# Performance work log

Hardware: AMD Instinct MI355X
Metric: run time of the kernel (lower is better)

## Reference

```python
import jax, jax.numpy as jnp
import numpy as np

DIM = 1024
HIDDEN = 2816
NUM_EXPERTS = 8
TOP_K = 2
BATCH, SEQ = 4, 2048


def setup_inputs() -> dict:
    key = jax.random.key(0)
    ks = jax.random.split(key, 5)
    x = jax.random.normal(ks[0], (BATCH, SEQ, DIM), dtype=jnp.float32)
    gate_w = jax.random.normal(ks[1], (NUM_EXPERTS, DIM), dtype=jnp.float32) * 0.02
    w1 = jax.random.normal(ks[2], (NUM_EXPERTS, HIDDEN, DIM), dtype=jnp.float32) * 0.02
    w3 = jax.random.normal(ks[3], (NUM_EXPERTS, HIDDEN, DIM), dtype=jnp.float32) * 0.02
    w2 = jax.random.normal(ks[4], (NUM_EXPERTS, DIM, HIDDEN), dtype=jnp.float32) * 0.02
    return {"x": x, "gate_w": gate_w, "w1": w1, "w3": w3, "w2": w2}


def reference(x, gate_w, w1, w3, w2):
    orig_shape = x.shape
    xf = x.reshape(-1, x.shape[-1])                      # [T, D]
    T = xf.shape[0]
    E, K = gate_w.shape[0], TOP_K

    # gating: softmax over experts, then top-k (descending, matches torch.topk)
    scores = jax.nn.softmax(xf @ gate_w.T, axis=-1)      # [T, E]
    expert_weights, expert_indices = jax.lax.top_k(scores, K)  # [T, K]
    expert_weights = expert_weights / jnp.sum(expert_weights, axis=-1, keepdims=True)

    # dispatch: each token duplicated K times (torch repeat_interleave)
    x_rep = jnp.repeat(xf, K, axis=0)                    # [T*K, D]
    flat_idx = expert_indices.reshape(-1)                # [T*K]

    # per-expert masked SwiGLU FFN, combined into y (loop over small fixed E)
    y = jnp.zeros_like(x_rep)
    for e in range(E):
        m = (flat_idx == e)[:, None]
        xe = jnp.where(m, x_rep, 0.0)                    # zero non-routed tokens
        h = jax.nn.silu(xe @ w1[e].T) * (xe @ w3[e].T)   # [T*K, H]
        out = h @ w2[e].T                                # [T*K, D]
        y = y + jnp.where(m, out, 0.0)

    # weighted combine over the K slots
    y = jnp.sum(y.reshape(T, K, -1) * expert_weights[..., None], axis=1)
    return y.reshape(orig_shape)
```

## Files before the change

### kernel.cpp

```cpp
#include <hip/hip_runtime.h>
#include <hip/hip_bf16.h>

#define NTOK 8192
#define DIM 1024
#define HID 2816
#define NE 8
#define NSLOT (NTOK*2)
#define BM 128
#define BK 32
#define MAXMT (NSLOT/BM + NE)

typedef float f32x4 __attribute__((ext_vector_type(4)));
typedef __bf16 bf16x8 __attribute__((ext_vector_type(8)));
typedef __bf16 bf16x4 __attribute__((ext_vector_type(4)));

#define MFMA(a,b,c) __builtin_amdgcn_mfma_f32_16x16x32_bf16(a,b,c,0,0,0)
#define SWZ(r,g) (((r)<<5) + ((((g) ^ (((r)>>1)&3)))<<3))

__device__ __forceinline__ void cvt_st8(__bf16* d, f32x4 a, f32x4 b){
  bf16x8 v;
  v[0]=(__bf16)a.x; v[1]=(__bf16)a.y; v[2]=(__bf16)a.z; v[3]=(__bf16)a.w;
  v[4]=(__bf16)b.x; v[5]=(__bf16)b.y; v[6]=(__bf16)b.z; v[7]=(__bf16)b.w;
  *reinterpret_cast<bf16x8*>(d) = v;
}
__device__ __forceinline__ void gld_lds16(const void* g, void* l){
  __builtin_amdgcn_global_load_lds(
    (const __attribute__((address_space(1))) void*)g,
    (__attribute__((address_space(3))) void*)l, 16, 0, 0);
}
__device__ __forceinline__ int xcd_map(int orig, int nwg){
  int q = nwg>>3, rr = nwg&7, x = orig&7, o = orig>>3;
  return (x<rr ? x*(q+1) : rr*(q+1)+(x-rr)*q) + o;
}

__global__ void k_zero(int* cnt){ if(threadIdx.x < NE) cnt[threadIdx.x] = 0; }

__global__ __launch_bounds__(256) void k_cvt3(
    const float* __restrict__ s1, const float* __restrict__ s3,
    const float* __restrict__ s2, __bf16* __restrict__ d1,
    __bf16* __restrict__ d3, __bf16* __restrict__ d2)
{
  const int PB = (NE*HID*DIM/8)/256;
  int seg = blockIdx.x / PB;
  int i   = (blockIdx.x % PB)*256 + threadIdx.x;
  const float* src = (seg==0) ? s1 : (seg==1) ? s3 : s2;
  __bf16*      dst = (seg==0) ? d1 : (seg==1) ? d3 : d2;
  const f32x4* s = reinterpret_cast<const f32x4*>(src) + (size_t)i*2;
  f32x4 a = s[0], b = s[1];
  cvt_st8(dst + (size_t)i*8, a, b);
}

__global__ __launch_bounds__(256) void k_gate(const float* __restrict__ x,
    const float* __restrict__ gw, int* __restrict__ idxs,
    float* __restrict__ wt, int* __restrict__ cnt, __bf16* __restrict__ xb)
{
  __shared__ double part[8][8][4];
  __shared__ double lg[8][8];

  int tid = threadIdx.x;
  int tl = tid>>5, e = (tid>>2)&7, q = tid&3;
  int t  = blockIdx.x*8 + tl;

  const f32x4* x4 = reinterpret_cast<const f32x4*>(x)  + (size_t)t*256 + q*64;
  const f32x4* g4 = reinterpret_cast<const f32x4*>(gw) + e*256 + q*64;

  double s0 = 0.0, s1 = 0.0;
#pragma unroll 4
  for(int j=0;j<64;j+=2){
    f32x4 a0 = x4[j],   b0 = g4[j];
    f32x4 a1 = x4[j+1], b1 = g4[j+1];
    s0 += (double)a0.x*b0.x + (double)a0.y*b0.y
        + (double)a0.z*b0.z + (double)a0.w*b0.w;
    s1 += (double)a1.x*b1.x + (double)a1.y*b1.y
        + (double)a1.z*b1.z + (double)a1.w*b1.w;
  }
  part[tl][e][q] = s0 + s1;
  __syncthreads();
  if(q==0)
    lg[tl][e] = part[tl][e][0] + part[tl][e][1] + part[tl][e][2] + part[tl][e][3];
  __syncthreads();

  if(tid < 8){
    int tt = blockIdx.x*8 + tid;
    int i1=0; double m1=lg[tid][0];
#pragma unroll
    for(int k=1;k<NE;k++) if(lg[tid][k]>m1){ m1=lg[tid][k]; i1=k; }
    int i2=-1; double m2=-1e300;
#pragma unroll
    for(int k=0;k<NE;k++) if(k!=i1 && lg[tid][k]>m2){ m2=lg[tid][k]; i2=k; }
    float e2 = __expf((float)(m2-m1));
    float w0 = 1.f/(1.f+e2);
    idxs[2*tt]=i1; idxs[2*tt+1]=i2;
    wt[2*tt]=w0;   wt[2*tt+1]=e2*w0;
    atomicAdd(&cnt[i1],1); atomicAdd(&cnt[i2],1);
  }

  const f32x4* xs = reinterpret_cast<const f32x4*>(x) + (size_t)blockIdx.x*2048;
  __bf16* xo = xb + (size_t)blockIdx.x*8192;
#pragma unroll
  for(int k=0;k<4;k++){
    int c = k*256 + tid;
    cvt_st8(xo + (size_t)c*8, xs[2*c], xs[2*c+1]);
  }
}

__global__ void k_prep(const int* __restrict__ cnt, int* __restrict__ off,
                       int* __restrict__ mtp, int* __restrict__ cursor)
{
  if(threadIdx.x==0){
    int o=0, m=0; off[0]=0; mtp[0]=0;
    for(int e=0;e<NE;e++){
      cursor[e]=o; o += cnt[e]; off[e+1]=o;
      m += (cnt[e]+BM-1)/BM;  mtp[e+1]=m;
    }
  }
}

__global__ __launch_bounds__(256) void k_scatter(const int* __restrict__ idxs,
    int* __restrict__ cursor, int* __restrict__ order, int* __restrict__ inv)
{
  int t = blockIdx.x*blockDim.x + threadIdx.x;
#pragma unroll
  for(int k=0;k<2;k++){
    int s = 2*t+k;
    int e = idxs[s];
    int p = atomicAdd(&cursor[e],1);
    order[p]=s; inv[s]=p;
  }
}

__global__ __launch_bounds__(512) void k_ffn1(
    const __bf16* __restrict__ xb, const __bf16* __restrict__ w1b,
    const __bf16* __restrict__ w3b, const int* __restrict__ off,
    const int* __restrict__ mtp, const int* __restrict__ order,
    __bf16* __restrict__ h)
{
  __shared__ __align__(16) __bf16 lA [2][BM*BK];
  __shared__ __align__(16) __bf16 lB1[2][BM*BK];
  __shared__ __align__(16) __bf16 lB3[2][BM*BK];

  const int NT = HID/128;
  int wg = xcd_map(blockIdx.x, MAXMT*NT);
  int mt = wg / NT, nt = wg % NT;
  if (mt >= mtp[NE]) return;
  int e = 0;
  while (mt >= mtp[e+1]) e++;
  int row0    = off[e] + (mt - mtp[e])*BM;
  int row_end = off[e+1];
  int n0      = nt*128;

  int tid = threadIdx.x, lane = tid&63;
  int srow = tid>>2;
  int scol = ((tid&3) ^ ((srow>>1)&3))<<3;
  int arow = min(row0 + srow, row_end-1);
  int tok  = order[arow] >> 1;
  const __bf16* gA  = xb  + (size_t)tok*DIM + scol;
  const __bf16* gB1 = w1b + (size_t)e*HID*DIM + (size_t)(n0+srow)*DIM + scol;
  const __bf16* gB3 = w3b + (size_t)e*HID*DIM + (size_t)(n0+srow)*DIM + scol;
  int ldso = (tid>>6)<<9;

  int wm = (tid>>6)>>2, wn = (tid>>6)&3;
  int fr = lane & 15, gq = lane>>4;

  f32x4 acc1[4][2], acc3[4][2];
#pragma unroll
  for(int m=0;m<4;m++)
#pragma unroll
    for(int n=0;n<2;n++){ acc1[m][n]=f32x4{0.f,0.f,0.f,0.f}; acc3[m][n]=f32x4{0.f,0.f,0.f,0.f}; }

  gld_lds16(gA,  &lA [0][ldso]);
  gld_lds16(gB1, &lB1[0][ldso]);
  gld_lds16(gB3, &lB3[0][ldso]);
  __syncthreads();

  const int NK = DIM/BK;
  int buf=0;
  for(int kt=0; kt<NK; kt++){
    if(kt+1<NK){
      gld_lds16(gA  + (kt+1)*BK, &lA [buf^1][ldso]);
      gld_lds16(gB1 + (kt+1)*BK, &lB1[buf^1][ldso]);
      gld_lds16(gB3 + (kt+1)*BK, &lB3[buf^1][ldso]);
    }
    bf16x8 av[4], bv[2], cv[2];
#pragma unroll
    for(int m=0;m<4;m++) av[m]=*reinterpret_cast<const bf16x8*>(&lA[buf][SWZ(wm*64+m*16+fr, gq)]);
#pragma unroll
    for(int n=0;n<2;n++){
      bv[n]=*reinterpret_cast<const bf16x8*>(&lB1[buf][SWZ(wn*32+n*16+fr, gq)]);
      cv[n]=*reinterpret_cast<const bf16x8*>(&lB3[buf][SWZ(wn*32+n*16+fr, gq)]);
    }
#pragma unroll
    for(int m=0;m<4;m++)
#pragma unroll
      for(int n=0;n<2;n++){
        acc1[m][n]=MFMA(av[m],bv[n],acc1[m][n]);
        acc3[m][n]=MFMA(av[m],cv[n],acc3[m][n]);
      }
    __syncthreads();
    buf^=1;
  }

#pragma unroll
  for(int m=0;m<4;m++){
    int rbase = row0 + wm*64 + m*16 + (gq<<2);
#pragma unroll
    for(int r=0;r<4;r++){
      if(rbase+r < row_end){
        __bf16* hp = h + (size_t)(rbase+r)*HID + n0 + wn*32 + fr;
#pragma unroll
        for(int n=0;n<2;n++){
          float u = acc1[m][n][r], v = acc3[m][n][r];
          hp[n*16] = (__bf16)( (u/(1.f+__expf(-u))) * v );
        }
      }
    }
  }
}

__global__ __launch_bounds__(256) void k_ffn2(
    const __bf16* __restrict__ h, const __bf16* __restrict__ w2b,
    const int* __restrict__ off, const int* __restrict__ mtp,
    __bf16* __restrict__ ys)
{
  __shared__ __align__(16) __bf16 lA[2][128*BK];
  __shared__ __align__(16) __bf16 lB[2][128*BK];

  const int NT = DIM/128;
  int wg = xcd_map(blockIdx.x, MAXMT*NT);
  int mt = wg / NT, nt = wg % NT;
  if (mt >= mtp[NE]) return;
  int e = 0;
  while (mt >= mtp[e+1]) e++;
  int row0    = off[e] + (mt - mtp[e])*BM;
  int row_end = off[e+1];
  int n0      = nt*128;

  int tid = threadIdx.x, lane = tid&63, wave = tid>>6;
  int srow = tid>>2;
  int scol = ((tid&3) ^ ((srow>>1)&3))<<3;
  int hr0 = min(row0 + srow,      NSLOT-1);
  int hr1 = min(row0 + srow + 64, NSLOT-1);
  const __bf16* gA0 = h   + (size_t)hr0*HID + scol;
  const __bf16* gA1 = h   + (size_t)hr1*HID + scol;
  const __bf16* gB0 = w2b + (size_t)e*DIM*HID + (size_t)(n0+srow)*HID + scol;
  const __bf16* gB1 = w2b + (size_t)e*DIM*HID + (size_t)(n0+srow+64)*HID + scol;
  int ldso = wave<<9;

  int wm = wave>>1, wn = wave&1;
  int fr = lane&15, gq = lane>>4;

  f32x4 acc[4][4];
#pragma unroll
  for(int m=0;m<4;m++)
#pragma unroll
    for(int n=0;n<4;n++) acc[m][n]=f32x4{0.f,0.f,0.f,0.f};

  gld_lds16(gA0, &lA[0][ldso]);
  gld_lds16(gA1, &lA[0][2048+ldso]);
  gld_lds16(gB0, &lB[0][ldso]);
  gld_lds16(gB1, &lB[0][2048+ldso]);
  __syncthreads();

  const int NK = HID/BK;
  int buf=0;
  for(int kt=0; kt<NK; kt++){
    if(kt+1<NK){
      gld_lds16(gA0 + (kt+1)*BK, &lA[buf^1][ldso]);
      gld_lds16(gA1 + (kt+1)*BK, &lA[buf^1][2048+ldso]);
      gld_lds16(gB0 + (kt+1)*BK, &lB[buf^1][ldso]);
      gld_lds16(gB1 + (kt+1)*BK, &lB[buf^1][2048+ldso]);
    }
    bf16x8 av[4], bv[4];
#pragma unroll
    for(int m=0;m<4;m++) av[m]=*reinterpret_cast<const bf16x8*>(&lA[buf][SWZ(wm*64+m*16+fr, gq)]);
#pragma unroll
    for(int n=0;n<4;n++) bv[n]=*reinterpret_cast<const bf16x8*>(&lB[buf][SWZ(wn*64+n*16+fr, gq)]);
#pragma unroll
    for(int m=0;m<4;m++)
#pragma unroll
      for(int n=0;n<4;n++)
        acc[m][n]=MFMA(av[m],bv[n],acc[m][n]);
    __syncthreads();
    buf^=1;
  }

#pragma unroll
  for(int m=0;m<4;m++){
    int rbase = row0 + wm*64 + m*16 + (gq<<2);
#pragma unroll
    for(int r=0;r<4;r++){
      if(rbase+r < row_end){
        __bf16* yp = ys + (size_t)(rbase+r)*DIM + n0 + wn*64 + fr;
#pragma unroll
        for(int n=0;n<4;n++) yp[n*16] = (__bf16)acc[m][n][r];
      }
    }
  }
}

__global__ __launch_bounds__(256) void k_combine(
    const __bf16* __restrict__ ys, const int* __restrict__ inv,
    const float* __restrict__ wt, float* __restrict__ y)
{
  int t  = blockIdx.x;
  int p0 = inv[2*t], p1 = inv[2*t+1];
  float w0 = wt[2*t], w1v = wt[2*t+1];
  int d = threadIdx.x*4;
  const __bf16* r0 = ys + (size_t)p0*DIM + d;
  const __bf16* r1 = ys + (size_t)p1*DIM + d;
  f32x4 o;
#pragma unroll
  for(int j=0;j<4;j++) o[j] = w0*(float)r0[j] + w1v*(float)r1[j];
  *reinterpret_cast<f32x4*>(y + (size_t)t*DIM + d) = o;
}

extern "C" void kernel_launch(void* const* d_in, const int* in_sizes, int n_in,
                              void* d_out, int out_size, void* d_ws, size_t ws_size,
                              hipStream_t stream)
{
  const float* x  = (const float*)d_in[0];
  const float* gw = (const float*)d_in[1];
  const float* w1 = (const float*)d_in[2];
  const float* w3 = (const float*)d_in[3];
  const float* w2 = (const float*)d_in[4];
  float* y = (float*)d_out;
  char* ws = (char*)d_ws;

  int*   cnt    = (int*)(ws + 0);
  int*   off    = (int*)(ws + 64);
  int*   mtp    = (int*)(ws + 128);
  int*   cursor = (int*)(ws + 256);
  int*   idxs   = (int*)(ws + 320);
  float* wt     = (float*)(ws + 320 + 65536);
  int*   order  = (int*)(ws + 320 + 2*65536);
  int*   inv    = (int*)(ws + 320 + 3*65536);
  __bf16* h     = (__bf16*)(ws + 262464);
  __bf16* xb    = (__bf16*)(ws + 262464 + 92274688ull);
  __bf16* w1b   = (__bf16*)(ws + 262464 + 92274688ull + 16777216ull);
  __bf16* w3b   = (__bf16*)(ws + 262464 + 92274688ull + 16777216ull + 46137344ull);
  __bf16* w2b   = (__bf16*)(ws + 262464 + 92274688ull + 16777216ull + 2*46137344ull);
  __bf16* ysb   = w1b;

  const int PB = (NE*HID*DIM/8)/256;

  k_zero   <<<1, 64, 0, stream>>>(cnt);
  k_gate   <<<NTOK/8, 256, 0, stream>>>(x, gw, idxs, wt, cnt, xb);
  k_prep   <<<1, 64, 0, stream>>>(cnt, off, mtp, cursor);
  k_scatter<<<NTOK/256, 256, 0, stream>>>(idxs, cursor, order, inv);
  k_cvt3   <<<3*PB, 256, 0, stream>>>(w1, w3, w2, w1b, w3b, w2b);
  k_ffn1   <<<MAXMT*(HID/128), 512, 0, stream>>>(xb, w1b, w3b, off, mtp, order, h);
  k_ffn2   <<<MAXMT*(DIM/128), 256, 0, stream>>>(h, w2b, off, mtp, ysb);
  k_combine<<<NTOK, 256, 0, stream>>>(ysb, inv, wt, y);
}
```

Before: 644.1 us.

## Triple-buffer ffn2 K-loop with vmcnt waits and split ffn1 into two launches

The down-projection GEMM moves from a double-buffered LDS pipeline with a full __syncthreads per step to a three-stage ring. It keeps two tile loads in flight and waits with s_waitcnt vmcnt plus a single barrier, so global-to-LDS latency can overlap more of the MFMA work. The gate/up GEMM is also split into two launches that each cover half of the 22 hidden column tiles, which changes workgroup ordering and L2 reuse of the expert weights. The ring adds LDS use in ffn2 and depends on hand-tuned waitcnt counts being correct, and the extra launch adds overhead.

```diff
diff --git a/kernel.cpp b/kernel.cpp
--- a/kernel.cpp
+++ b/kernel.cpp
@@ -16,6 +16,7 @@
 
 #define MFMA(a,b,c) __builtin_amdgcn_mfma_f32_16x16x32_bf16(a,b,c,0,0,0)
 #define SWZ(r,g) (((r)<<5) + ((((g) ^ (((r)>>1)&3)))<<3))
+#define VMW(N) asm volatile("s_waitcnt vmcnt(" #N ")" ::: "memory")
 
 __device__ __forceinline__ void cvt_st8(__bf16* d, f32x4 a, f32x4 b){
   bf16x8 v;
@@ -129,19 +130,19 @@
   }
 }
 
+#define NT_H 11
 __global__ __launch_bounds__(512) void k_ffn1(
     const __bf16* __restrict__ xb, const __bf16* __restrict__ w1b,
     const __bf16* __restrict__ w3b, const int* __restrict__ off,
     const int* __restrict__ mtp, const int* __restrict__ order,
-    __bf16* __restrict__ h)
+    __bf16* __restrict__ h, int nt_off)
 {
   __shared__ __align__(16) __bf16 lA [2][BM*BK];
   __shared__ __align__(16) __bf16 lB1[2][BM*BK];
   __shared__ __align__(16) __bf16 lB3[2][BM*BK];
 
-  const int NT = HID/128;
-  int wg = xcd_map(blockIdx.x, MAXMT*NT);
-  int mt = wg / NT, nt = wg % NT;
+  int wg = xcd_map(blockIdx.x, MAXMT*NT_H);
+  int mt = wg / NT_H, nt = nt_off + wg % NT_H;
   if (mt >= mtp[NE]) return;
   int e = 0;
   while (mt >= mtp[e+1]) e++;
@@ -222,8 +223,8 @@
     const int* __restrict__ off, const int* __restrict__ mtp,
     __bf16* __restrict__ ys)
 {
-  __shared__ __align__(16) __bf16 lA[2][128*BK];
-  __shared__ __align__(16) __bf16 lB[2][128*BK];
+  __shared__ __align__(16) __bf16 lA[3][128*BK];
+  __shared__ __align__(16) __bf16 lB[3][128*BK];
 
   const int NT = DIM/128;
   int wg = xcd_map(blockIdx.x, MAXMT*NT);
@@ -255,34 +256,39 @@
 #pragma unroll
     for(int n=0;n<4;n++) acc[m][n]=f32x4{0.f,0.f,0.f,0.f};
 
-  gld_lds16(gA0, &lA[0][ldso]);
-  gld_lds16(gA1, &lA[0][2048+ldso]);
-  gld_lds16(gB0, &lB[0][ldso]);
-  gld_lds16(gB1, &lB[0][2048+ldso]);
-  __syncthreads();
+#define F2_STG(b, kt_) { \
+    gld_lds16(gA0 + (kt_)*BK, &lA[b][ldso]); \
+    gld_lds16(gA1 + (kt_)*BK, &lA[b][2048+ldso]); \
+    gld_lds16(gB0 + (kt_)*BK, &lB[b][ldso]); \
+    gld_lds16(gB1 + (kt_)*BK, &lB[b][2048+ldso]); }
+
+#define F2_CMP(b) { \
+    bf16x8 av[4], bv[4]; \
+    _Pragma("unroll") for(int m_=0;m_<4;m_++) \
+      av[m_]=*reinterpret_cast<const bf16x8*>(&lA[b][SWZ(wm*64+m_*16+fr, gq)]); \
+    _Pragma("unroll") for(int n_=0;n_<4;n_++) \
+      bv[n_]=*reinterpret_cast<const bf16x8*>(&lB[b][SWZ(wn*64+n_*16+fr, gq)]); \
+    _Pragma("unroll") for(int m_=0;m_<4;m_++) _Pragma("unroll") for(int n_=0;n_<4;n_++) \
+      acc[m_][n_]=MFMA(av[m_],bv[n_],acc[m_][n_]); }
+
+  F2_STG(0,0);
+  F2_STG(1,1);
 
   const int NK = HID/BK;
-  int buf=0;
-  for(int kt=0; kt<NK; kt++){
-    if(kt+1<NK){
-      gld_lds16(gA0 + (kt+1)*BK, &lA[buf^1][ldso]);
-      gld_lds16(gA1 + (kt+1)*BK, &lA[buf^1][2048+ldso]);
-      gld_lds16(gB0 + (kt+1)*BK, &lB[buf^1][ldso]);
-      gld_lds16(gB1 + (kt+1)*BK, &lB[buf^1][2048+ldso]);
-    }
-    bf16x8 av[4], bv[4];
-#pragma unroll
-    for(int m=0;m<4;m++) av[m]=*reinterpret_cast<const bf16x8*>(&lA[buf][SWZ(wm*64+m*16+fr, gq)]);
-#pragma unroll
-    for(int n=0;n<4;n++) bv[n]=*reinterpret_cast<const bf16x8*>(&lB[buf][SWZ(wn*64+n*16+fr, gq)]);
-#pragma unroll
-    for(int m=0;m<4;m++)
-#pragma unroll
-      for(int n=0;n<4;n++)
-        acc[m][n]=MFMA(av[m],bv[n],acc[m][n]);
-    __syncthreads();
-    buf^=1;
-  }
+  for(int kt=0; kt<NK-1; ++kt){
+    VMW(4);
+    __builtin_amdgcn_s_barrier();
+    asm volatile("" ::: "memory");
+    if(kt+2 < NK) F2_STG((kt+2)%3, kt+2);
+    F2_CMP(kt%3);
+  }
+  VMW(0);
+  __builtin_amdgcn_s_barrier();
+  asm volatile("" ::: "memory");
+  F2_CMP((NK-1)%3);
+
+#undef F2_STG
+#undef F2_CMP
 
 #pragma unroll
   for(int m=0;m<4;m++){
@@ -348,7 +354,8 @@
   k_prep   <<<1, 64, 0, stream>>>(cnt, off, mtp, cursor);
   k_scatter<<<NTOK/256, 256, 0, stream>>>(idxs, cursor, order, inv);
   k_cvt3   <<<3*PB, 256, 0, stream>>>(w1, w3, w2, w1b, w3b, w2b);
-  k_ffn1   <<<MAXMT*(HID/128), 512, 0, stream>>>(xb, w1b, w3b, off, mtp, order, h);
+  k_ffn1   <<<MAXMT*NT_H, 512, 0, stream>>>(xb, w1b, w3b, off, mtp, order, h, 0);
+  k_ffn1   <<<MAXMT*NT_H, 512, 0, stream>>>(xb, w1b, w3b, off, mtp, order, h, NT_H);
   k_ffn2   <<<MAXMT*(DIM/128), 256, 0, stream>>>(h, w2b, off, mtp, ysb);
   k_combine<<<NTOK, 256, 0, stream>>>(ysb, inv, wt, y);
 }
```

New measurement: 651.5 us. No clear change (+1.1%).

## Fuse weighted combine into FFN2 epilogue via atomic adds and drop zero kernel

Applied to the files above, without the earlier changes.

The separate combine kernel and its bf16 intermediate buffer are removed. The FFN2 epilogue now scales each row by its routing weight and atomically adds it into the fp32 output, which the gate kernel zeroes first. Counter zeroing moves into the weight-conversion kernel, so two launches disappear. The cost is a float atomic per output element, plus nondeterministic summation order, in exchange for skipping the intermediate write and read.

```diff
diff --git a/kernel.cpp b/kernel.cpp
--- a/kernel.cpp
+++ b/kernel.cpp
@@ -33,13 +33,12 @@
   return (x<rr ? x*(q+1) : rr*(q+1)+(x-rr)*q) + o;
 }
 
-__global__ void k_zero(int* cnt){ if(threadIdx.x < NE) cnt[threadIdx.x] = 0; }
-
 __global__ __launch_bounds__(256) void k_cvt3(
     const float* __restrict__ s1, const float* __restrict__ s3,
     const float* __restrict__ s2, __bf16* __restrict__ d1,
-    __bf16* __restrict__ d3, __bf16* __restrict__ d2)
-{
+    __bf16* __restrict__ d3, __bf16* __restrict__ d2, int* __restrict__ cnt)
+{
+  if(blockIdx.x==0 && threadIdx.x < NE) cnt[threadIdx.x] = 0;
   const int PB = (NE*HID*DIM/8)/256;
   int seg = blockIdx.x / PB;
   int i   = (blockIdx.x % PB)*256 + threadIdx.x;
@@ -52,7 +51,8 @@
 
 __global__ __launch_bounds__(256) void k_gate(const float* __restrict__ x,
     const float* __restrict__ gw, int* __restrict__ idxs,
-    float* __restrict__ wt, int* __restrict__ cnt, __bf16* __restrict__ xb)
+    float* __restrict__ wt, int* __restrict__ cnt, __bf16* __restrict__ xb,
+    float* __restrict__ y)
 {
   __shared__ double part[8][8][4];
   __shared__ double lg[8][8];
@@ -102,6 +102,11 @@
     int c = k*256 + tid;
     cvt_st8(xo + (size_t)c*8, xs[2*c], xs[2*c+1]);
   }
+
+  f32x4* yz = reinterpret_cast<f32x4*>(y) + (size_t)blockIdx.x*2048;
+#pragma unroll
+  for(int k=0;k<8;k++)
+    yz[k*256 + tid] = f32x4{0.f,0.f,0.f,0.f};
 }
 
 __global__ void k_prep(const int* __restrict__ cnt, int* __restrict__ off,
@@ -117,7 +122,7 @@
 }
 
 __global__ __launch_bounds__(256) void k_scatter(const int* __restrict__ idxs,
-    int* __restrict__ cursor, int* __restrict__ order, int* __restrict__ inv)
+    int* __restrict__ cursor, int* __restrict__ order)
 {
   int t = blockIdx.x*blockDim.x + threadIdx.x;
 #pragma unroll
@@ -125,7 +130,7 @@
     int s = 2*t+k;
     int e = idxs[s];
     int p = atomicAdd(&cursor[e],1);
-    order[p]=s; inv[s]=p;
+    order[p]=s;
   }
 }
 
@@ -220,7 +225,8 @@
 __global__ __launch_bounds__(256) void k_ffn2(
     const __bf16* __restrict__ h, const __bf16* __restrict__ w2b,
     const int* __restrict__ off, const int* __restrict__ mtp,
-    __bf16* __restrict__ ys)
+    const int* __restrict__ order, const float* __restrict__ wt,
+    float* __restrict__ y)
 {
   __shared__ __align__(16) __bf16 lA[2][128*BK];
   __shared__ __align__(16) __bf16 lB[2][128*BK];
@@ -289,29 +295,16 @@
     int rbase = row0 + wm*64 + m*16 + (gq<<2);
 #pragma unroll
     for(int r=0;r<4;r++){
-      if(rbase+r < row_end){
-        __bf16* yp = ys + (size_t)(rbase+r)*DIM + n0 + wn*64 + fr;
-#pragma unroll
-        for(int n=0;n<4;n++) yp[n*16] = (__bf16)acc[m][n][r];
+      int p = rbase + r;
+      if(p < row_end){
+        int s = order[p];
+        float wv = wt[s];
+        float* yp = y + (size_t)(s>>1)*DIM + n0 + wn*64 + fr;
+#pragma unroll
+        for(int n=0;n<4;n++) atomicAdd(&yp[n*16], wv*acc[m][n][r]);
       }
     }
   }
-}
-
-__global__ __launch_bounds__(256) void k_combine(
-    const __bf16* __restrict__ ys, const int* __restrict__ inv,
-    const float* __restrict__ wt, float* __restrict__ y)
-{
-  int t  = blockIdx.x;
-  int p0 = inv[2*t], p1 = inv[2*t+1];
-  float w0 = wt[2*t], w1v = wt[2*t+1];
-  int d = threadIdx.x*4;
-  const __bf16* r0 = ys + (size_t)p0*DIM + d;
-  const __bf16* r1 = ys + (size_t)p1*DIM + d;
-  f32x4 o;
-#pragma unroll
-  for(int j=0;j<4;j++) o[j] = w0*(float)r0[j] + w1v*(float)r1[j];
-  *reinterpret_cast<f32x4*>(y + (size_t)t*DIM + d) = o;
 }
 
 extern "C" void kernel_launch(void* const* d_in, const int* in_sizes, int n_in,
@@ -333,22 +326,18 @@
   int*   idxs   = (int*)(ws + 320);
   float* wt     = (float*)(ws + 320 + 65536);
   int*   order  = (int*)(ws + 320 + 2*65536);
-  int*   inv    = (int*)(ws + 320 + 3*65536);
   __bf16* h     = (__bf16*)(ws + 262464);
   __bf16* xb    = (__bf16*)(ws + 262464 + 92274688ull);
   __bf16* w1b   = (__bf16*)(ws + 262464 + 92274688ull + 16777216ull);
   __bf16* w3b   = (__bf16*)(ws + 262464 + 92274688ull + 16777216ull + 46137344ull);
   __bf16* w2b   = (__bf16*)(ws + 262464 + 92274688ull + 16777216ull + 2*46137344ull);
-  __bf16* ysb   = w1b;
 
   const int PB = (NE*HID*DIM/8)/256;
 
-  k_zero   <<<1, 64, 0, stream>>>(cnt);
-  k_gate   <<<NTOK/8, 256, 0, stream>>>(x, gw, idxs, wt, cnt, xb);
+  k_cvt3   <<<3*PB, 256, 0, stream>>>(w1, w3, w2, w1b, w3b, w2b, cnt);
+  k_gate   <<<NTOK/8, 256, 0, stream>>>(x, gw, idxs, wt, cnt, xb, y);
   k_prep   <<<1, 64, 0, stream>>>(cnt, off, mtp, cursor);
-  k_scatter<<<NTOK/256, 256, 0, stream>>>(idxs, cursor, order, inv);
-  k_cvt3   <<<3*PB, 256, 0, stream>>>(w1, w3, w2, w1b, w3b, w2b);
+  k_scatter<<<NTOK/256, 256, 0, stream>>>(idxs, cursor, order);
   k_ffn1   <<<MAXMT*(HID/128), 512, 0, stream>>>(xb, w1b, w3b, off, mtp, order, h);
-  k_ffn2   <<<MAXMT*(DIM/128), 256, 0, stream>>>(h, w2b, off, mtp, ysb);
-  k_combine<<<NTOK, 256, 0, stream>>>(ysb, inv, wt, y);
-}
+  k_ffn2   <<<MAXMT*(DIM/128), 256, 0, stream>>>(h, w2b, off, mtp, order, wt, y);
+}
```

Result: no change. 656.4 us (+1.9%).
